# Performance work log

Measured on AMD Instinct MI355X. Metric: run time of the kernel, lower is better.

The kernel has to match this reference:

```python
import jax, jax.numpy as jnp
import numpy as np

B, S, D, H, EXP = 4, 2048, 768, 8, 4
HD = D // H  # head dim = 96
EPS = 1e-5


def layer_norm(x, g, b):
    mu = jnp.mean(x, axis=-1, keepdims=True)
    var = jnp.mean(jnp.square(x - mu), axis=-1, keepdims=True)
    return (x - mu) * jax.lax.rsqrt(var + EPS) * g + b


def setup_inputs() -> dict:
    key = jax.random.key(0)
    ks = jax.random.split(key, 16)
    s = 0.02
    f32 = jnp.float32
    x = jax.random.normal(ks[0], (B, S, D), f32)
    Wq = jax.random.normal(ks[1], (D, D), f32) * s
    bq = jnp.zeros((D,), f32)
    Wk = jax.random.normal(ks[2], (D, D), f32) * s
    bk = jnp.zeros((D,), f32)
    Wv = jax.random.normal(ks[3], (D, D), f32) * s
    bv = jnp.zeros((D,), f32)
    Wo = jax.random.normal(ks[4], (D, D), f32) * s
    bo = jnp.zeros((D,), f32)
    g1 = jnp.ones((D,), f32)
    be1 = jnp.zeros((D,), f32)
    W1 = jax.random.normal(ks[5], (D, D * EXP), f32) * s
    bf1 = jnp.zeros((D * EXP,), f32)
    W2 = jax.random.normal(ks[6], (D * EXP, D), f32) * s
    bf2 = jnp.zeros((D,), f32)
    g2 = jnp.ones((D,), f32)
    be2 = jnp.zeros((D,), f32)
    return dict(x=x, Wq=Wq, bq=bq, Wk=Wk, bk=bk, Wv=Wv, bv=bv, Wo=Wo, bo=bo,
                g1=g1, be1=be1, W1=W1, bf1=bf1, W2=W2, bf2=bf2, g2=g2, be2=be2)


def reference(x, Wq, bq, Wk, bk, Wv, bv, Wo, bo, g1, be1, W1, bf1, W2, bf2, g2, be2):
    scale = HD ** (-0.5)
    # multi-head attention (manual QK^T softmax V)
    q = (x @ Wq + bq).reshape(B, S, H, HD).transpose(0, 2, 1, 3)  # b H s c
    k = (x @ Wk + bk).reshape(B, S, H, HD).transpose(0, 2, 1, 3)
    v = (x @ Wv + bv).reshape(B, S, H, HD).transpose(0, 2, 1, 3)
    scores = jnp.einsum('bhqc,bhkc->bhqk', q, k) * scale
    attn = jax.nn.softmax(scores, axis=-1)
    o = jnp.einsum('bhqk,bhkc->bhqc', attn, v)
    o = o.transpose(0, 2, 1, 3).reshape(B, S, D)
    attn_out = o @ Wo + bo
    # residual + LN
    x1 = layer_norm(attn_out + x, g1, be1)
    # feed-forward with GELU
    h = jax.nn.gelu(x1 @ W1 + bf1)
    ffn_out = h @ W2 + bf2
    # residual + LN
    return layer_norm(ffn_out + x1, g2, be2)
```

## Files before the change

### kernel.cpp

```cpp
#include <hip/hip_runtime.h>
#include <hip/hip_bf16.h>
#include <math.h>
#include <stdint.h>

#define B_    4
#define S_    2048
#define D_    768
#define H_    8
#define HD_   96
#define EXPD_ 3072
#define MSZ   8192

#define QSCALE 0.14724439f
#define M0_    12.0f

typedef __bf16 bf16;
typedef __bf16 bf16x4 __attribute__((ext_vector_type(4)));
typedef __bf16 bf16x8 __attribute__((ext_vector_type(8)));
typedef float  f32x4  __attribute__((ext_vector_type(4)));
typedef float  f32x16 __attribute__((ext_vector_type(16)));

typedef __attribute__((address_space(1))) const uint32_t gu32;
typedef __attribute__((address_space(3))) uint32_t lu32;

__device__ __forceinline__ void async_copy16(const void* g, void* l) {
    __builtin_amdgcn_global_load_lds((gu32*)g, (lu32*)l, 16, 0, 0);
}

template<int N> __device__ __forceinline__ void vm_wait() {
    if constexpr (N == 0)      asm volatile("s_waitcnt vmcnt(0)" ::: "memory");
    else if constexpr (N == 3) asm volatile("s_waitcnt vmcnt(3)" ::: "memory");
    else if constexpr (N == 4) asm volatile("s_waitcnt vmcnt(4)" ::: "memory");
    else static_assert(N == 0 || N == 3 || N == 4, "unsupported vmcnt");
}

__device__ __forceinline__ float gelu_f(float x) {
    float x3 = x * x * x;
    return 0.5f * x * (1.0f + tanhf(0.7978845608028654f * (x + 0.044715f * x3)));
}

__device__ __forceinline__ bool sniff_f32(const void* p) {
    const bf16* pb = (const bf16*)p;
    float v = (float)pb[2 * (threadIdx.x & 63)];
    bool big = !(fabsf(v) < 1000.0f);
    return __any(big) != 0;
}

__device__ __forceinline__ float dynld(const void* p, size_t i, bool f32in) {
    return f32in ? ((const float*)p)[i] : (float)((const bf16*)p)[i];
}

__global__ __launch_bounds__(256) void cast_kernel(
    const void* __restrict__ src, bf16* __restrict__ dst)
{
    const bool f32in = sniff_f32(src);
    size_t i = ((size_t)blockIdx.x * 256 + threadIdx.x) * 8;
    if (f32in) {
        f32x4 a = *(const f32x4*)((const float*)src + i);
        f32x4 b = *(const f32x4*)((const float*)src + i + 4);
        bf16x8 r;
#pragma unroll
        for (int e = 0; e < 4; ++e) { r[e] = (bf16)a[e]; r[e + 4] = (bf16)b[e]; }
        *(bf16x8*)(dst + i) = r;
    } else {
        *(bf16x8*)(dst + i) = *(const bf16x8*)((const bf16*)src + i);
    }
}

#define MODE_QKV  0
#define MODE_RES  1
#define MODE_GELU 2

template<int MODE, bool ADYN, bool RESDYN, int BN>
__global__ __launch_bounds__(256) void gemm2_kernel(
    const void* __restrict__ A, const bf16* __restrict__ Bt,
    const void* __restrict__ b0, const void* __restrict__ b1, const void* __restrict__ b2,
    const void* __restrict__ res, bf16* __restrict__ out,
    int M, int N, int K, int lda, int ldb, int boff, int mstripe,
    const void* __restrict__ sniffp)
{
    constexpr int WN   = BN / 2;
    constexpr int NJ32 = WN / 32;
    constexpr int ABUF = 4096;
    constexpr int BBUF = BN * 32;
    constexpr int BUF  = ABUF + BBUF;
    __shared__ __align__(16) bf16 Sh[2 * BUF];

    const bool f32in = sniff_f32(sniffp);
    const int tid  = threadIdx.x;
    const int w    = tid >> 6;
    const int lane = tid & 63;
    const int l32  = lane & 31;
    const int kh   = lane >> 5;
    const int wr   = w >> 1, wc = w & 1;

    const int lin  = blockIdx.x;
    const int xcd  = lin & 7;
    const int q    = lin >> 3;
    const int nb   = q / mstripe;
    const int mbin = q - nb * mstripe;
    const int m0   = (xcd * mstripe + mbin) * 128;
    const int n0   = nb * BN;

    const int rsub = lane >> 2;
    const int cswz = (((lane & 3) ^ ((rsub >> 1) & 3))) * 8;
    const int xh   = (l32 >> 1) & 3;

    f32x16 acc[2][NJ32];
#pragma unroll
    for (int i = 0; i < 2; ++i)
#pragma unroll
        for (int j = 0; j < NJ32; ++j)
#pragma unroll
            for (int e = 0; e < 16; ++e) acc[i][j][e] = 0.f;

    const bf16*  Abf = (const bf16*)A;
    const float* Af  = (const float*)A;

    auto stage = [&](int k0, int bsel) {
        bf16* As = Sh + bsel * BUF;
        bf16* Bs = As + ABUF;
#pragma unroll
        for (int p = 0; p < 2; ++p) {
            int row = p * 64 + w * 16;
            async_copy16(Abf + (size_t)(m0 + row + rsub) * lda + k0 + cswz,
                         &As[row * 32]);
        }
#pragma unroll
        for (int p = 0; p < BN / 64; ++p) {
            int row = p * 64 + w * 16;
            async_copy16(Bt + (size_t)(n0 + row + rsub) * ldb + k0 + cswz,
                         &Bs[row * 32]);
        }
    };

    auto compute = [&](int bsel) {
        const bf16* As = Sh + bsel * BUF;
        const bf16* Bs = As + ABUF;
        bf16x8 af[2][2], bfv[NJ32][2];
#pragma unroll
        for (int i = 0; i < 2; ++i)
#pragma unroll
            for (int ks = 0; ks < 2; ++ks)
                af[i][ks] = *(const bf16x8*)(&As[(wr * 64 + i * 32 + l32) * 32
                                                + (((ks * 2 + kh) ^ xh) * 8)]);
#pragma unroll
        for (int j = 0; j < NJ32; ++j)
#pragma unroll
            for (int ks = 0; ks < 2; ++ks)
                bfv[j][ks] = *(const bf16x8*)(&Bs[(wc * WN + j * 32 + l32) * 32
                                                  + (((ks * 2 + kh) ^ xh) * 8)]);
        asm volatile("s_waitcnt lgkmcnt(0)" ::: "memory");
        __builtin_amdgcn_sched_barrier(0);
        __builtin_amdgcn_s_setprio(1);
#pragma unroll
        for (int i = 0; i < 2; ++i)
#pragma unroll
            for (int j = 0; j < NJ32; ++j)
#pragma unroll
                for (int ks = 0; ks < 2; ++ks)
                    acc[i][j] = __builtin_amdgcn_mfma_f32_32x32x16_bf16(af[i][ks], bfv[j][ks], acc[i][j], 0, 0, 0);
        __builtin_amdgcn_s_setprio(0);
    };

    const int nk = K >> 5;
    if constexpr (ADYN) {
        auto stage_adyn = [&](int k0, int bsel) {
            bf16* As = Sh + bsel * BUF;
            bf16* Bs = As + ABUF;
            if (f32in) {
#pragma unroll
                for (int p = 0; p < 2; ++p) {
                    int row = p * 64 + w * 16 + rsub;
                    const float* sp = Af + (size_t)(m0 + row) * lda + k0 + cswz;
                    f32x4 u0 = *(const f32x4*)sp;
                    f32x4 u1 = *(const f32x4*)(sp + 4);
                    bf16x8 v;
#pragma unroll
                    for (int e = 0; e < 4; ++e) { v[e] = (bf16)u0[e]; v[e + 4] = (bf16)u1[e]; }
                    *(bf16x8*)(&As[row * 32 + (lane & 3) * 8]) = v;
                }
            } else {
#pragma unroll
                for (int p = 0; p < 2; ++p) {
                    int row = p * 64 + w * 16;
                    async_copy16(Abf + (size_t)(m0 + row + rsub) * lda + k0 + cswz,
                                 &As[row * 32]);
                }
            }
#pragma unroll
            for (int p = 0; p < BN / 64; ++p) {
                int row = p * 64 + w * 16;
                async_copy16(Bt + (size_t)(n0 + row + rsub) * ldb + k0 + cswz,
                             &Bs[row * 32]);
            }
        };
        stage_adyn(0, 0);
        __syncthreads();
        for (int t = 0; t < nk; ++t) {
            const int cur = t & 1;
            if (t + 1 < nk) stage_adyn((t + 1) << 5, cur ^ 1);
            compute(cur);
            __syncthreads();
        }
    } else {
        stage(0, 0);
        vm_wait<0>();
        __builtin_amdgcn_s_barrier();
        for (int t = 0; t < nk; ++t) {
            const int cur = t & 1;
            if (t + 1 < nk) stage((t + 1) << 5, cur ^ 1);
            compute(cur);
            vm_wait<0>();
            __builtin_amdgcn_s_barrier();
        }
    }
    __syncthreads();

    if constexpr (MODE == MODE_QKV) {
        bf16* Cw = Sh + w * 2048;
        const int bb = (m0 + wr * 64) >> 11;
#pragma unroll
        for (int j = 0; j < NJ32; ++j) {
            int nbase = n0 + wc * WN + j * 32;
            int which = nbase / D_;
            int n2b   = nbase - which * D_;
            int h     = n2b / HD_;
            int hd0   = n2b - h * HD_;
            const void* bp = which == 0 ? b0 : (which == 1 ? b1 : b2);
            float bval = dynld(bp, n2b + l32, f32in);
            const int bh = bb * H_ + h;
#pragma unroll
            for (int i = 0; i < 2; ++i)
#pragma unroll
                for (int g = 0; g < 16; ++g) {
                    int rr = (g & 3) + 8 * (g >> 2) + 4 * kh;
                    float v = acc[i][j][g] + bval;
                    if (which == 0) v *= QSCALE;
                    Cw[(i * 32 + rr) * 32 + l32] = (bf16)v;
                }
            if (which < 2) {
#pragma unroll
                for (int pass = 0; pass < 4; ++pass) {
                    int row = pass * 16 + (lane >> 2);
                    int c8  = (lane & 3) * 8;
                    bf16x8 cv = *(const bf16x8*)&Cw[row * 32 + c8];
                    int ss = (m0 + wr * 64 + row) & (S_ - 1);
                    size_t dst = (size_t)which * (MSZ * D_) + ((size_t)bh * S_ + ss) * HD_ + hd0 + c8;
                    *(bf16x8*)&out[dst] = cv;
                }
            } else {
                int hd  = hd0 + l32;
                int ss0 = (m0 + wr * 64) & (S_ - 1);
                size_t rowb = (size_t)2 * (MSZ * D_) + ((size_t)bh * HD_ + hd) * S_ + ss0 + kh * 32;
#pragma unroll
                for (int oct = 0; oct < 4; ++oct) {
                    bf16x8 cv;
#pragma unroll
                    for (int e = 0; e < 8; ++e)
                        cv[e] = Cw[(kh * 32 + oct * 8 + e) * 32 + l32];
                    *(bf16x8*)&out[rowb + oct * 8] = cv;
                }
            }
        }
    } else {
        bf16* Cw = Sh + w * 2048;
        for (int j = 0; j < NJ32; ++j) {
            int nl = n0 + wc * WN + j * 32 + l32;
            float bval = boff >= 0 ? dynld(b0, boff + nl, f32in) : 0.f;
#pragma unroll
            for (int i = 0; i < 2; ++i)
#pragma unroll
                for (int g = 0; g < 16; ++g) {
                    int rr = (g & 3) + 8 * (g >> 2) + 4 * kh;
                    float v = acc[i][j][g] + bval;
                    if constexpr (MODE == MODE_GELU) v = gelu_f(v);
                    Cw[(i * 32 + rr) * 32 + l32] = (bf16)v;
                }
#pragma unroll
            for (int pass = 0; pass < 4; ++pass) {
                int row = pass * 16 + (lane >> 2);
                int cc  = (lane & 3) * 8;
                bf16x8 cv = *(const bf16x8*)&Cw[row * 32 + cc];
                int m = m0 + wr * 64 + row;
                int n = n0 + wc * WN + j * 32 + cc;
                size_t off = (size_t)m * N + n;
                if constexpr (MODE == MODE_RES) {
                    bf16x8 o;
                    if (RESDYN && f32in) {
                        f32x4 r0 = *(const f32x4*)((const float*)res + off);
                        f32x4 r1 = *(const f32x4*)((const float*)res + off + 4);
#pragma unroll
                        for (int e = 0; e < 4; ++e) {
                            o[e]     = (bf16)((float)cv[e] + r0[e]);
                            o[e + 4] = (bf16)((float)cv[e + 4] + r1[e]);
                        }
                    } else {
                        bf16x8 rv = *(const bf16x8*)((const bf16*)res + off);
#pragma unroll
                        for (int e = 0; e < 8; ++e) o[e] = (bf16)((float)cv[e] + (float)rv[e]);
                    }
                    *(bf16x8*)&out[off] = o;
                } else {
                    *(bf16x8*)&out[off] = cv;
                }
            }
        }
    }
}

__global__ __launch_bounds__(256, 2) void flash_kernel(
    const bf16* __restrict__ Q, const bf16* __restrict__ Kk,
    const bf16* __restrict__ Vt_g, bf16* __restrict__ ctx)
{
    __shared__ __align__(16) bf16 Ks[64][104];
    __shared__ __align__(16) bf16 Vs[96][72];
    __shared__ __align__(16) bf16 Ps[4][32][72];

    const int tid  = threadIdx.x;
    const int w    = tid >> 6;
    const int lane = tid & 63;
    const int quad = lane >> 4;
    const int l16  = lane & 15;
    const int bh   = blockIdx.x;
    const size_t base = (size_t)bh * S_ * HD_;
    const int q0   = blockIdx.y * 128 + w * 32;

    bf16x8 qf[2][3];
#pragma unroll
    for (int qs = 0; qs < 2; ++qs)
#pragma unroll
        for (int ch = 0; ch < 3; ++ch)
            qf[qs][ch] = *(const bf16x8*)(Q + base + (size_t)(q0 + qs * 16 + l16) * HD_ + ch * 32 + quad * 8);

    f32x4 oacc[2][6];
#pragma unroll
    for (int qs = 0; qs < 2; ++qs)
#pragma unroll
        for (int c = 0; c < 6; ++c) oacc[qs][c] = (f32x4){0.f, 0.f, 0.f, 0.f};
    float lsum[2] = {0.f, 0.f};

    int krow[3], kc8[3], vrow[3], vc8[3];
#pragma unroll
    for (int i = 0; i < 3; ++i) {
        int id = tid + i * 256;
        krow[i] = id / 12; kc8[i] = (id - krow[i] * 12) * 8;
        vrow[i] = id >> 3; vc8[i] = (id & 7) * 8;
    }

    bf16x8 kreg[3], vreg[3];
#pragma unroll
    for (int i = 0; i < 3; ++i) {
        kreg[i] = *(const bf16x8*)(Kk + base + (size_t)krow[i] * HD_ + kc8[i]);
        vreg[i] = *(const bf16x8*)(Vt_g + base + (size_t)vrow[i] * S_ + vc8[i]);
    }
#pragma unroll
    for (int i = 0; i < 3; ++i) {
        *(bf16x8*)(&Ks[krow[i]][kc8[i]]) = kreg[i];
        *(bf16x8*)(&Vs[vrow[i]][vc8[i]]) = vreg[i];
    }
    __syncthreads();

    for (int kv0 = 0; kv0 < S_; kv0 += 64) {
        const bool more = (kv0 + 64) < S_;
        if (more) {
#pragma unroll
            for (int i = 0; i < 3; ++i) {
                kreg[i] = *(const bf16x8*)(Kk + base + (size_t)(kv0 + 64 + krow[i]) * HD_ + kc8[i]);
                vreg[i] = *(const bf16x8*)(Vt_g + base + (size_t)vrow[i] * S_ + kv0 + 64 + vc8[i]);
            }
        }

        f32x4 sacc[2][4];
#pragma unroll
        for (int qs = 0; qs < 2; ++qs)
#pragma unroll
            for (int t = 0; t < 4; ++t)
                sacc[qs][t] = (f32x4){-M0_, -M0_, -M0_, -M0_};
#pragma unroll
        for (int t = 0; t < 4; ++t)
#pragma unroll
            for (int ch = 0; ch < 3; ++ch) {
                bf16x8 kf = *(const bf16x8*)(&Ks[t * 16 + l16][ch * 32 + quad * 8]);
                sacc[0][t] = __builtin_amdgcn_mfma_f32_16x16x32_bf16(kf, qf[0][ch], sacc[0][t], 0, 0, 0);
                sacc[1][t] = __builtin_amdgcn_mfma_f32_16x16x32_bf16(kf, qf[1][ch], sacc[1][t], 0, 0, 0);
            }

#pragma unroll
        for (int qs = 0; qs < 2; ++qs) {
            bf16* prow = &Ps[w][qs * 16 + l16][quad * 4];
#pragma unroll
            for (int t = 0; t < 4; ++t) {
                float p0 = exp2f(sacc[qs][t][0]);
                float p1 = exp2f(sacc[qs][t][1]);
                float p2 = exp2f(sacc[qs][t][2]);
                float p3 = exp2f(sacc[qs][t][3]);
                lsum[qs] += (p0 + p1) + (p2 + p3);
                bf16x4 pv;
                pv[0] = (bf16)p0; pv[1] = (bf16)p1; pv[2] = (bf16)p2; pv[3] = (bf16)p3;
                *(bf16x4*)(prow + t * 16) = pv;
            }
        }

        bf16x8 pf[2][2];
#pragma unroll
        for (int qs = 0; qs < 2; ++qs) {
            pf[qs][0] = *(const bf16x8*)(&Ps[w][qs * 16 + l16][quad * 8]);
            pf[qs][1] = *(const bf16x8*)(&Ps[w][qs * 16 + l16][32 + quad * 8]);
        }
#pragma unroll
        for (int c = 0; c < 6; ++c) {
            bf16x8 vf0 = *(const bf16x8*)(&Vs[c * 16 + l16][quad * 8]);
            bf16x8 vf1 = *(const bf16x8*)(&Vs[c * 16 + l16][32 + quad * 8]);
            oacc[0][c] = __builtin_amdgcn_mfma_f32_16x16x32_bf16(pf[0][0], vf0, oacc[0][c], 0, 0, 0);
            oacc[0][c] = __builtin_amdgcn_mfma_f32_16x16x32_bf16(pf[0][1], vf1, oacc[0][c], 0, 0, 0);
            oacc[1][c] = __builtin_amdgcn_mfma_f32_16x16x32_bf16(pf[1][0], vf0, oacc[1][c], 0, 0, 0);
            oacc[1][c] = __builtin_amdgcn_mfma_f32_16x16x32_bf16(pf[1][1], vf1, oacc[1][c], 0, 0, 0);
        }

        if (more) {
            __syncthreads();
#pragma unroll
            for (int i = 0; i < 3; ++i) {
                *(bf16x8*)(&Ks[krow[i]][kc8[i]]) = kreg[i];
                *(bf16x8*)(&Vs[vrow[i]][vc8[i]]) = vreg[i];
            }
            __syncthreads();
        }
    }

#pragma unroll
    for (int qs = 0; qs < 2; ++qs) {
        lsum[qs] += __shfl_xor(lsum[qs], 16);
        lsum[qs] += __shfl_xor(lsum[qs], 32);
    }
    const int b = bh >> 3, h = bh & 7;
#pragma unroll
    for (int qs = 0; qs < 2; ++qs)
#pragma unroll
        for (int r = 0; r < 4; ++r) {
            float inv = 1.0f / __shfl(lsum[qs], quad * 4 + r);
            int srow = q0 + qs * 16 + quad * 4 + r;
            size_t rowbase = ((size_t)b * S_ + srow) * D_ + h * HD_;
#pragma unroll
            for (int c = 0; c < 6; ++c)
                ctx[rowbase + c * 16 + l16] = (bf16)(oacc[qs][c][r] * inv);
        }
}

template<bool OUTDYN>
__global__ __launch_bounds__(256) void ln_kernel(
    const bf16* __restrict__ in, const void* __restrict__ g, const void* __restrict__ be,
    void* __restrict__ out, const void* __restrict__ sniffp)
{
    const bool f32in = sniff_f32(sniffp);
    const int w = threadIdx.x >> 6, lane = threadIdx.x & 63;
    const int row = blockIdx.x * 4 + w;
    const size_t rbase = (size_t)row * D_ + lane * 12;

    float v[12];
#pragma unroll
    for (int j = 0; j < 3; ++j) {
        bf16x4 t = *(const bf16x4*)(in + rbase + j * 4);
#pragma unroll
        for (int e = 0; e < 4; ++e) v[j * 4 + e] = (float)t[e];
    }
    float sum = 0.f;
#pragma unroll
    for (int j = 0; j < 12; ++j) sum += v[j];
#pragma unroll
    for (int off = 1; off < 64; off <<= 1) sum += __shfl_xor(sum, off);
    float mu = sum * (1.0f / D_);
    float sq = 0.f;
#pragma unroll
    for (int j = 0; j < 12; ++j) { v[j] -= mu; sq += v[j] * v[j]; }
#pragma unroll
    for (int off = 1; off < 64; off <<= 1) sq += __shfl_xor(sq, off);
    float rstd = rsqrtf(sq * (1.0f / D_) + 1e-5f);

    if (OUTDYN && f32in) {
        float* op = (float*)out + rbase;
#pragma unroll
        for (int j = 0; j < 3; ++j) {
            f32x4 t;
#pragma unroll
            for (int e = 0; e < 4; ++e) {
                int c = lane * 12 + j * 4 + e;
                t[e] = v[j * 4 + e] * rstd * dynld(g, c, true) + dynld(be, c, true);
            }
            *(f32x4*)(op + j * 4) = t;
        }
    } else {
        bf16* op = (bf16*)out + rbase;
#pragma unroll
        for (int j = 0; j < 3; ++j) {
            bf16x4 t;
#pragma unroll
            for (int e = 0; e < 4; ++e) {
                int c = lane * 12 + j * 4 + e;
                t[e] = (bf16)(v[j * 4 + e] * rstd * dynld(g, c, f32in) + dynld(be, c, f32in));
            }
            *(bf16x4*)(op + j * 4) = t;
        }
    }
}

__device__ __forceinline__ void transpose_tile(
    const void* __restrict__ src, bf16* __restrict__ dst, int R, int C,
    int r0, int c0, bool f32in)
{
    __shared__ bf16 t[64][65];
    const int tx = threadIdx.x & 63, ty = threadIdx.x >> 6;
#pragma unroll
    for (int i = 0; i < 16; ++i) {
        int rr = ty + i * 4;
        t[rr][tx] = (bf16)dynld(src, (size_t)(r0 + rr) * C + c0 + tx, f32in);
    }
    __syncthreads();
#pragma unroll
    for (int i = 0; i < 16; ++i) {
        int cc = ty + i * 4;
        dst[(size_t)(c0 + cc) * R + r0 + tx] = t[tx][cc];
    }
}

__global__ __launch_bounds__(256) void transpose_qkv_kernel(
    const void* __restrict__ s0, const void* __restrict__ s1, const void* __restrict__ s2,
    bf16* __restrict__ dst)
{
    const void* src = blockIdx.z == 0 ? s0 : (blockIdx.z == 1 ? s1 : s2);
    const bool f32in = sniff_f32(src);
    transpose_tile(src, dst + (size_t)blockIdx.z * D_ * D_, D_, D_,
                   blockIdx.y * 64, blockIdx.x * 64, f32in);
}

__global__ __launch_bounds__(256) void transpose_mlp_kernel(
    const void* __restrict__ s0, const void* __restrict__ s1, const void* __restrict__ s2,
    bf16* __restrict__ dst)
{
    int id = blockIdx.x;
    const void* src;
    int R, C, r, c;
    size_t off;
    if (id < 144)      { src = s0; R = D_;    C = D_;    off = 0;
                         r = id / 12;          c = id % 12; }
    else if (id < 720) { src = s1; R = D_;    C = EXPD_; off = (size_t)D_ * D_;
                         int i = id - 144;     r = i / 48; c = i % 48; }
    else               { src = s2; R = EXPD_; C = D_;    off = (size_t)D_ * D_ + (size_t)D_ * EXPD_;
                         int i = id - 720;     r = i / 12; c = i % 12; }
    const bool f32in = sniff_f32(src);
    transpose_tile(src, dst + off, R, C, r * 64, c * 64, f32in);
}

extern "C" void kernel_launch(void* const* d_in, const int* in_sizes, int n_in,
                              void* d_out, int out_size, void* d_ws, size_t ws_size,
                              hipStream_t stream)
{
    (void)in_sizes; (void)n_in; (void)out_size;
    const void* x   = d_in[0];
    const void* Wq  = d_in[1];
    const void* bq  = d_in[2];
    const void* Wk  = d_in[3];
    const void* bk  = d_in[4];
    const void* Wv  = d_in[5];
    const void* bv  = d_in[6];
    const void* Wo  = d_in[7];
    const void* bo  = d_in[8];
    const void* g1  = d_in[9];
    const void* be1 = d_in[10];
    const void* W1  = d_in[11];
    const void* bf1 = d_in[12];
    const void* W2  = d_in[13];
    const void* bf2 = d_in[14];
    const void* g2  = d_in[15];
    const void* be2 = d_in[16];

    const size_t REG = (size_t)MSZ * D_ * 2;
    char* p = (char*)d_ws;
    bf16* R0 = (bf16*)p;
    bf16* R1 = (bf16*)(p + REG);
    bf16* R2 = (bf16*)(p + 2 * REG);
    bf16* R3 = (bf16*)(p + 3 * REG);
    bf16* R4 = (bf16*)(p + 4 * REG);

    int tier = 0;
    if      (ws_size >= 9 * REG) tier = 3;
    else if (ws_size >= 5 * REG) tier = 1;
    bf16* xb = tier == 3 ? (bf16*)(p + 8 * REG) : R4;

    bf16* qkvT = (bf16*)d_out;
    bf16* ctx  = (bf16*)d_out;
    dim3 blk(256);
    const int MB8 = MSZ / 128 / 8;

    if (tier >= 1) cast_kernel<<<dim3(MSZ * D_ / (256 * 8)), blk, 0, stream>>>(x, xb);

    transpose_qkv_kernel<<<dim3(12, 12, 3), blk, 0, stream>>>(Wq, Wk, Wv, qkvT);

    if (tier >= 1)
        gemm2_kernel<MODE_QKV, false, false, 128><<<dim3(64 * 18), blk, 0, stream>>>(
            xb, qkvT, bq, bk, bv, nullptr, R0, MSZ, 2304, D_, D_, D_, 0, MB8, Wq);
    else
        gemm2_kernel<MODE_QKV, true, false, 128><<<dim3(64 * 18), blk, 0, stream>>>(
            x, qkvT, bq, bk, bv, nullptr, R0, MSZ, 2304, D_, D_, D_, 0, MB8, Wq);

    flash_kernel<<<dim3(B_ * H_, S_ / 128), dim3(256), 0, stream>>>(R0, R1, R2, ctx);

    bf16* WoT = R1;
    bf16* W1T = WoT + (size_t)D_ * D_;
    bf16* W2T = W1T + (size_t)D_ * EXPD_;
    transpose_mlp_kernel<<<dim3(1296), blk, 0, stream>>>(Wo, W1, W2, WoT);

    if (tier >= 1)
        gemm2_kernel<MODE_RES, false, false, 64><<<dim3(64 * 12), blk, 0, stream>>>(
            ctx, WoT, bo, nullptr, nullptr, xb, R3, MSZ, D_, D_, D_, D_, 0, MB8, Wq);
    else
        gemm2_kernel<MODE_RES, false, true, 64><<<dim3(64 * 12), blk, 0, stream>>>(
            ctx, WoT, bo, nullptr, nullptr, x, R3, MSZ, D_, D_, D_, D_, 0, MB8, Wq);

    bf16* x1b = R0;
    ln_kernel<false><<<dim3(MSZ / 4), blk, 0, stream>>>(R3, g1, be1, x1b, Wq);

    bf16* y2b;
    if (tier == 3) {
        bf16* hb = R4;
        y2b = R3;
        gemm2_kernel<MODE_GELU, false, false, 128><<<dim3(64 * 24), blk, 0, stream>>>(
            x1b, W1T, bf1, nullptr, nullptr, nullptr, hb, MSZ, EXPD_, D_, D_, D_, 0, MB8, Wq);
        gemm2_kernel<MODE_RES, false, false, 64><<<dim3(64 * 12), blk, 0, stream>>>(
            hb, W2T, bf2, nullptr, nullptr, x1b, y2b, MSZ, D_, EXPD_, EXPD_, EXPD_, 0, MB8, Wq);
    } else if (tier == 1) {
        bf16* hb = R2;
        y2b = R4;
        gemm2_kernel<MODE_GELU, false, false, 128><<<dim3(64 * 12), blk, 0, stream>>>(
            x1b, W1T, bf1, nullptr, nullptr, nullptr, hb, MSZ, 1536, D_, D_, D_, 0, MB8, Wq);
        gemm2_kernel<MODE_RES, false, false, 64><<<dim3(64 * 12), blk, 0, stream>>>(
            hb, W2T, bf2, nullptr, nullptr, x1b, y2b, MSZ, D_, 1536, 1536, EXPD_, 0, MB8, Wq);
        gemm2_kernel<MODE_GELU, false, false, 128><<<dim3(64 * 12), blk, 0, stream>>>(
            x1b, W1T + (size_t)1536 * D_, bf1, nullptr, nullptr, nullptr, hb, MSZ, 1536, D_, D_, D_, 1536, MB8, Wq);
        gemm2_kernel<MODE_RES, false, false, 64><<<dim3(64 * 12), blk, 0, stream>>>(
            hb, W2T + 1536, nullptr, nullptr, nullptr, y2b, y2b, MSZ, D_, 1536, 1536, EXPD_, -1, MB8, Wq);
    } else {
        bf16* hb = R3;
        y2b = R2;
        const int CH = 2048;
        for (int c0 = 0; c0 < MSZ; c0 += CH) {
            const bf16* x1c = x1b + (size_t)c0 * D_;
            gemm2_kernel<MODE_GELU, false, false, 128><<<dim3(16 * 24), blk, 0, stream>>>(
                x1c, W1T, bf1, nullptr, nullptr, nullptr, hb, CH, EXPD_, D_, D_, D_, 0, 2, Wq);
            gemm2_kernel<MODE_RES, false, false, 64><<<dim3(16 * 12), blk, 0, stream>>>(
                hb, W2T, bf2, nullptr, nullptr, x1c, y2b + (size_t)c0 * D_, CH, D_, EXPD_, EXPD_, EXPD_, 0, 2, Wq);
        }
    }

    ln_kernel<true><<<dim3(MSZ / 4), blk, 0, stream>>>(y2b, g2, be2, d_out, Wq);
}
```

Measured before the change: 431.0 us.

## Split attention KV range across two blocks and fuse prep kernels into one launch

Flash attention now splits the KV sequence into two halves on a third grid dimension when workspace allows. Each half writes unnormalized fp32 partial outputs and row sums, and a new combine kernel adds them and normalizes. This doubles the attention grid from 256 blocks to fill the GPU better, at the cost of extra fp32 traffic and one more launch. The input cast, QKV weight transpose and (when the output buffer is large) the MLP weight transpose are merged into one prep kernel to cut launch count. The split relies on a fixed softmax offset (M0) rather than a running max, which is what makes adding the partials directly valid.

Measured after the change: 443.0 us. 2.8% more time.

```diff
diff --git a/kernel.cpp b/kernel.cpp
--- a/kernel.cpp
+++ b/kernel.cpp
@@ -50,20 +50,68 @@
     return f32in ? ((const float*)p)[i] : (float)((const bf16*)p)[i];
 }
 
-__global__ __launch_bounds__(256) void cast_kernel(
-    const void* __restrict__ src, bf16* __restrict__ dst)
+__device__ __forceinline__ void transpose_tile(
+    const void* __restrict__ src, bf16* __restrict__ dst, int R, int C,
+    int r0, int c0, bool f32in)
 {
-    const bool f32in = sniff_f32(src);
-    size_t i = ((size_t)blockIdx.x * 256 + threadIdx.x) * 8;
-    if (f32in) {
-        f32x4 a = *(const f32x4*)((const float*)src + i);
-        f32x4 b = *(const f32x4*)((const float*)src + i + 4);
-        bf16x8 r;
-#pragma unroll
-        for (int e = 0; e < 4; ++e) { r[e] = (bf16)a[e]; r[e + 4] = (bf16)b[e]; }
-        *(bf16x8*)(dst + i) = r;
-    } else {
-        *(bf16x8*)(dst + i) = *(const bf16x8*)((const bf16*)src + i);
+    __shared__ bf16 t[64][65];
+    const int tx = threadIdx.x & 63, ty = threadIdx.x >> 6;
+#pragma unroll
+    for (int i = 0; i < 16; ++i) {
+        int rr = ty + i * 4;
+        t[rr][tx] = (bf16)dynld(src, (size_t)(r0 + rr) * C + c0 + tx, f32in);
+    }
+    __syncthreads();
+#pragma unroll
+    for (int i = 0; i < 16; ++i) {
+        int cc = ty + i * 4;
+        dst[(size_t)(c0 + cc) * R + r0 + tx] = t[tx][cc];
+    }
+}
+
+__global__ __launch_bounds__(256) void prep_kernel(
+    const void* __restrict__ x, bf16* __restrict__ xb, int nCast,
+    const void* __restrict__ Wq, const void* __restrict__ Wk, const void* __restrict__ Wv,
+    bf16* __restrict__ qkvT,
+    const void* __restrict__ Wo, const void* __restrict__ W1, const void* __restrict__ W2,
+    bf16* __restrict__ mlpT)
+{
+    int id = blockIdx.x;
+    if (id < nCast) {
+        const bool f32in = sniff_f32(x);
+        size_t i = ((size_t)id * 256 + threadIdx.x) * 8;
+        if (f32in) {
+            f32x4 a = *(const f32x4*)((const float*)x + i);
+            f32x4 b = *(const f32x4*)((const float*)x + i + 4);
+            bf16x8 r;
+#pragma unroll
+            for (int e = 0; e < 4; ++e) { r[e] = (bf16)a[e]; r[e + 4] = (bf16)b[e]; }
+            *(bf16x8*)(xb + i) = r;
+        } else {
+            *(bf16x8*)(xb + i) = *(const bf16x8*)((const bf16*)x + i);
+        }
+        return;
+    }
+    id -= nCast;
+    if (id < 432) {
+        int z = id / 144, rem = id - z * 144;
+        const void* src = z == 0 ? Wq : (z == 1 ? Wk : Wv);
+        const bool f32in = sniff_f32(src);
+        transpose_tile(src, qkvT + (size_t)z * D_ * D_, D_, D_,
+                       (rem / 12) * 64, (rem % 12) * 64, f32in);
+        return;
+    }
+    id -= 432;
+    {
+        const void* src; int R, C, r, c; size_t off;
+        if (id < 144)      { src = Wo; R = D_;    C = D_;    off = 0;
+                             r = id / 12;          c = id % 12; }
+        else if (id < 720) { src = W1; R = D_;    C = EXPD_; off = (size_t)D_ * D_;
+                             int i = id - 144;     r = i / 48; c = i % 48; }
+        else               { src = W2; R = EXPD_; C = D_;    off = (size_t)D_ * D_ + (size_t)D_ * EXPD_;
+                             int i = id - 720;     r = i / 12; c = i % 12; }
+        const bool f32in = sniff_f32(src);
+        transpose_tile(src, mlpT + off, R, C, r * 64, c * 64, f32in);
     }
 }
 
@@ -309,9 +357,11 @@
     }
 }
 
+template<bool SPLIT>
 __global__ __launch_bounds__(256, 2) void flash_kernel(
     const bf16* __restrict__ Q, const bf16* __restrict__ Kk,
-    const bf16* __restrict__ Vt_g, bf16* __restrict__ ctx)
+    const bf16* __restrict__ Vt_g, bf16* __restrict__ ctx,
+    float* __restrict__ opart, float* __restrict__ lsums)
 {
     __shared__ __align__(16) bf16 Ks[64][104];
     __shared__ __align__(16) bf16 Vs[96][72];
@@ -323,6 +373,9 @@
     const int quad = lane >> 4;
     const int l16  = lane & 15;
     const int bh   = blockIdx.x;
+    const int g    = SPLIT ? blockIdx.z : 0;
+    const int kvlo = SPLIT ? g * (S_ / 2) : 0;
+    const int kvhi = SPLIT ? kvlo + S_ / 2 : S_;
     const size_t base = (size_t)bh * S_ * HD_;
     const int q0   = blockIdx.y * 128 + w * 32;
 
@@ -351,8 +404,8 @@
     bf16x8 kreg[3], vreg[3];
 #pragma unroll
     for (int i = 0; i < 3; ++i) {
-        kreg[i] = *(const bf16x8*)(Kk + base + (size_t)krow[i] * HD_ + kc8[i]);
-        vreg[i] = *(const bf16x8*)(Vt_g + base + (size_t)vrow[i] * S_ + vc8[i]);
+        kreg[i] = *(const bf16x8*)(Kk + base + (size_t)(kvlo + krow[i]) * HD_ + kc8[i]);
+        vreg[i] = *(const bf16x8*)(Vt_g + base + (size_t)vrow[i] * S_ + kvlo + vc8[i]);
     }
 #pragma unroll
     for (int i = 0; i < 3; ++i) {
@@ -361,8 +414,8 @@
     }
     __syncthreads();
 
-    for (int kv0 = 0; kv0 < S_; kv0 += 64) {
-        const bool more = (kv0 + 64) < S_;
+    for (int kv0 = kvlo; kv0 < kvhi; kv0 += 64) {
+        const bool more = (kv0 + 64) < kvhi;
         if (more) {
 #pragma unroll
             for (int i = 0; i < 3; ++i) {
@@ -435,17 +488,59 @@
         lsum[qs] += __shfl_xor(lsum[qs], 32);
     }
     const int b = bh >> 3, h = bh & 7;
-#pragma unroll
-    for (int qs = 0; qs < 2; ++qs)
-#pragma unroll
-        for (int r = 0; r < 4; ++r) {
-            float inv = 1.0f / __shfl(lsum[qs], quad * 4 + r);
-            int srow = q0 + qs * 16 + quad * 4 + r;
-            size_t rowbase = ((size_t)b * S_ + srow) * D_ + h * HD_;
-#pragma unroll
-            for (int c = 0; c < 6; ++c)
-                ctx[rowbase + c * 16 + l16] = (bf16)(oacc[qs][c][r] * inv);
-        }
+    if constexpr (SPLIT) {
+        float* op = opart + (size_t)g * ((size_t)MSZ * D_);
+#pragma unroll
+        for (int qs = 0; qs < 2; ++qs) {
+            if (quad == 0)
+                lsums[((size_t)g * B_ * H_ + bh) * S_ + q0 + qs * 16 + l16] = lsum[qs];
+#pragma unroll
+            for (int r = 0; r < 4; ++r) {
+                int srow = q0 + qs * 16 + quad * 4 + r;
+                size_t rowbase = ((size_t)b * S_ + srow) * D_ + h * HD_;
+#pragma unroll
+                for (int c = 0; c < 6; ++c)
+                    op[rowbase + c * 16 + l16] = oacc[qs][c][r];
+            }
+        }
+    } else {
+#pragma unroll
+        for (int qs = 0; qs < 2; ++qs)
+#pragma unroll
+            for (int r = 0; r < 4; ++r) {
+                float inv = 1.0f / __shfl(lsum[qs], quad * 4 + r);
+                int srow = q0 + qs * 16 + quad * 4 + r;
+                size_t rowbase = ((size_t)b * S_ + srow) * D_ + h * HD_;
+#pragma unroll
+                for (int c = 0; c < 6; ++c)
+                    ctx[rowbase + c * 16 + l16] = (bf16)(oacc[qs][c][r] * inv);
+            }
+    }
+}
+
+__global__ __launch_bounds__(256) void combine_kernel(
+    const float* __restrict__ o0, const float* __restrict__ o1,
+    const float* __restrict__ ls, bf16* __restrict__ ctx)
+{
+    int idx = blockIdx.x * 256 + threadIdx.x;
+    int row = idx / 96;
+    int ch  = idx - row * 96;
+    int col = ch * 8;
+    int h   = col / HD_;
+    size_t li = ((size_t)(row >> 11) * H_ + h) * S_ + (row & (S_ - 1));
+    float inv = 1.0f / (ls[li] + ls[(size_t)B_ * H_ * S_ + li]);
+    size_t off = (size_t)row * D_ + col;
+    f32x4 a0 = *(const f32x4*)(o0 + off);
+    f32x4 a1 = *(const f32x4*)(o0 + off + 4);
+    f32x4 c0 = *(const f32x4*)(o1 + off);
+    f32x4 c1 = *(const f32x4*)(o1 + off + 4);
+    bf16x8 r;
+#pragma unroll
+    for (int e = 0; e < 4; ++e) {
+        r[e]     = (bf16)((a0[e] + c0[e]) * inv);
+        r[e + 4] = (bf16)((a1[e] + c1[e]) * inv);
+    }
+    *(bf16x8*)(ctx + off) = r;
 }
 
 template<bool OUTDYN>
@@ -503,35 +598,6 @@
             *(bf16x4*)(op + j * 4) = t;
         }
     }
-}
-
-__device__ __forceinline__ void transpose_tile(
-    const void* __restrict__ src, bf16* __restrict__ dst, int R, int C,
-    int r0, int c0, bool f32in)
-{
-    __shared__ bf16 t[64][65];
-    const int tx = threadIdx.x & 63, ty = threadIdx.x >> 6;
-#pragma unroll
-    for (int i = 0; i < 16; ++i) {
-        int rr = ty + i * 4;
-        t[rr][tx] = (bf16)dynld(src, (size_t)(r0 + rr) * C + c0 + tx, f32in);
-    }
-    __syncthreads();
-#pragma unroll
-    for (int i = 0; i < 16; ++i) {
-        int cc = ty + i * 4;
-        dst[(size_t)(c0 + cc) * R + r0 + tx] = t[tx][cc];
-    }
-}
-
-__global__ __launch_bounds__(256) void transpose_qkv_kernel(
-    const void* __restrict__ s0, const void* __restrict__ s1, const void* __restrict__ s2,
-    bf16* __restrict__ dst)
-{
-    const void* src = blockIdx.z == 0 ? s0 : (blockIdx.z == 1 ? s1 : s2);
-    const bool f32in = sniff_f32(src);
-    transpose_tile(src, dst + (size_t)blockIdx.z * D_ * D_, D_, D_,
-                   blockIdx.y * 64, blockIdx.x * 64, f32in);
 }
 
 __global__ __launch_bounds__(256) void transpose_mlp_kernel(
@@ -556,7 +622,7 @@
                               void* d_out, int out_size, void* d_ws, size_t ws_size,
                               hipStream_t stream)
 {
-    (void)in_sizes; (void)n_in; (void)out_size;
+    (void)in_sizes; (void)n_in;
     const void* x   = d_in[0];
     const void* Wq  = d_in[1];
     const void* bq  = d_in[2];
@@ -590,12 +656,16 @@
 
     bf16* qkvT = (bf16*)d_out;
     bf16* ctx  = (bf16*)d_out;
+    const size_t MLPT_B = (size_t)(D_ * D_ + 2 * D_ * EXPD_) * 2;
+    const bool bigOut = (size_t)out_size >= (size_t)MSZ * D_ * 2 + MLPT_B + (1 << 20);
+    bf16* mlpT = bigOut ? (bf16*)((char*)d_out + (size_t)out_size - MLPT_B) : R1;
+
     dim3 blk(256);
     const int MB8 = MSZ / 128 / 8;
-
-    if (tier >= 1) cast_kernel<<<dim3(MSZ * D_ / (256 * 8)), blk, 0, stream>>>(x, xb);
-
-    transpose_qkv_kernel<<<dim3(12, 12, 3), blk, 0, stream>>>(Wq, Wk, Wv, qkvT);
+    const int nCast = tier >= 1 ? MSZ * D_ / (256 * 8) : 0;
+
+    prep_kernel<<<dim3(nCast + 432 + (bigOut ? 1296 : 0)), blk, 0, stream>>>(
+        x, xb, nCast, Wq, Wk, Wv, qkvT, Wo, W1, W2, mlpT);
 
     if (tier >= 1)
         gemm2_kernel<MODE_QKV, false, false, 128><<<dim3(64 * 18), blk, 0, stream>>>(
@@ -604,12 +674,24 @@
         gemm2_kernel<MODE_QKV, true, false, 128><<<dim3(64 * 18), blk, 0, stream>>>(
             x, qkvT, bq, bk, bv, nullptr, R0, MSZ, 2304, D_, D_, D_, 0, MB8, Wq);
 
-    flash_kernel<<<dim3(B_ * H_, S_ / 128), dim3(256), 0, stream>>>(R0, R1, R2, ctx);
-
-    bf16* WoT = R1;
+    if (tier == 3) {
+        float* o0 = (float*)(p + 4 * REG);
+        float* o1 = o0 + (size_t)MSZ * D_;
+        float* ls = (float*)R3;
+        flash_kernel<true><<<dim3(B_ * H_, S_ / 128, 2), dim3(256), 0, stream>>>(
+            R0, R1, R2, nullptr, o0, ls);
+        combine_kernel<<<dim3(MSZ * 96 / 256), blk, 0, stream>>>(o0, o1, ls, ctx);
+    } else {
+        flash_kernel<false><<<dim3(B_ * H_, S_ / 128), dim3(256), 0, stream>>>(
+            R0, R1, R2, ctx, nullptr, nullptr);
+    }
+
+    if (!bigOut)
+        transpose_mlp_kernel<<<dim3(1296), blk, 0, stream>>>(Wo, W1, W2, mlpT);
+
+    bf16* WoT = mlpT;
     bf16* W1T = WoT + (size_t)D_ * D_;
     bf16* W2T = W1T + (size_t)D_ * EXPD_;
-    transpose_mlp_kernel<<<dim3(1296), blk, 0, stream>>>(Wo, W1, W2, WoT);
 
     if (tier >= 1)
         gemm2_kernel<MODE_RES, false, false, 64><<<dim3(64 * 12), blk, 0, stream>>>(
```
